# Optimization experiments

Measured on AMD Instinct MI355X. Metric: run time of the kernel, lower is better.

Reference implementation:

```python
import jax, jax.numpy as jnp
import numpy as np

# ---- model constants (match init_kwargs) ----
B, N = 128, 4096                 # N_BATCH, N_NEURON
N_STEPS, N_STEADY, N_WINDOW = 200, 100, 20
V_THRESH, V_REST = 1.0, 0.0
DT, TAU, TAU_SYN = 0.01, 0.02, 0.02
EXP_DT_TAU = float(np.exp(-DT / TAU))
DT_TAU = DT / TAU
EXP_DT_TAU_SYN = float(np.exp(-DT / TAU_SYN))
DT_TAU_SYN = DT / TAU_SYN

# recording schedule: steps >= N_STEADY with step % N_WINDOW == 0
REC_IDX = np.arange(N_STEADY, N_STEPS, N_WINDOW)                     # [100,120,140,160,180]
PREV_IDX = np.concatenate([[N_STEADY - N_WINDOW - 1], REC_IDX[:-1]])  # window starts (exclusive)


def setup_inputs() -> dict:
    key = jax.random.key(0)
    k1, k2, k3 = jax.random.split(key, 3)
    # feedforward drive with a positive baseline so the net actually spikes
    ff_input = 0.5 + 0.3 * jax.random.normal(k1, (B, N_STEPS, N), jnp.float32)
    # recurrent weights (transposed, as in torch: spikes @ Wab_T)
    Wab_T = jax.random.normal(k2, (N, N), jnp.float32) / np.sqrt(N)
    # initial synaptic recurrent input (torch initVolt uses randn)
    rec0 = jax.random.normal(k3, (B, N), jnp.float32)
    return {"ff_input": ff_input, "Wab_T": Wab_T, "rec0": rec0}


def reference(ff_input, Wab_T, rec0):
    dtype = ff_input.dtype
    volts0 = jnp.zeros((B, N), dtype)
    spikes0 = jnp.zeros((B, N), dtype)  # volts=0 < V_THRESH -> no initial spikes

    def step(carry, ff_t):
        volts, rec, spikes = carry
        hidden = spikes @ Wab_T                              # [B,N] GEMM
        rec = rec * EXP_DT_TAU_SYN + hidden * DT_TAU_SYN     # synaptic decay (SYN_DYN)
        volts = volts * EXP_DT_TAU + DT_TAU * (ff_t + rec)   # LIF voltage update
        spk = volts >= V_THRESH
        volts = jnp.where(spk, V_REST, volts)                # masked reset
        spikes = spk.astype(dtype)
        return (volts, rec, spikes), (spikes, volts)

    _, (spk_all, v_all) = jax.lax.scan(
        step, (volts0, rec0, spikes0), jnp.swapaxes(ff_input, 0, 1)
    )  # spk_all, v_all: [N_STEPS, B, N]

    # windowed moving averages, matching torch accumulate/reset logic
    cs_s = jnp.cumsum(spk_all, axis=0)
    cs_v = jnp.cumsum(v_all, axis=0)
    rates = (cs_s[REC_IDX] - cs_s[PREV_IDX]) / N_WINDOW      # [5, B, N]
    volts_avg = (cs_v[REC_IDX] - cs_v[PREV_IDX]) / N_WINDOW
    spikes_rec = spk_all[REC_IDX]

    return (
        jnp.swapaxes(rates, 0, 1),       # [B, 5, N]
        jnp.swapaxes(volts_avg, 0, 1),   # [B, 5, N]
        jnp.swapaxes(spikes_rec, 0, 1),  # [B, 5, N]
    )
```

## Files before the change

kernel.cpp:

```cpp
#include <hip/hip_runtime.h>
#include <stdint.h>

#define NBATCH 128
#define NNEUR  4096
#define TLAST  180
#define DECAY  0.6065306597126334f

__global__ __launch_bounds__(256) void lif_step(
    const float* __restrict__ ff, const float* __restrict__ W,
    const float* __restrict__ rec0, float* __restrict__ out,
    float* __restrict__ volts, float* __restrict__ rec,
    float* __restrict__ sum_s, float* __restrict__ sum_v,
    const unsigned long long* __restrict__ bits_old,
    unsigned long long* __restrict__ bits_new, int t)
{
#pragma clang fp contract(off)
    __shared__ __align__(16) unsigned short slist[NNEUR];
    __shared__ int scnt;

    const int tid  = threadIdx.x;
    const int lane = tid & 63;
    const int wid  = tid >> 6;
    const int bid  = blockIdx.x;
    const int b    = bid >> 3;
    const int tile = bid & 7;
    const int c0   = (tile << 9) + (wid << 7);
    const int n0   = c0 + (lane << 1);
    const unsigned laneb = (unsigned)n0 * 4u;

    float accx = 0.f, accy = 0.f;

    if (t > 0) {
        if (wid == 0) {
            unsigned long long m = bits_old[(b << 6) + lane];
            int c = __popcll(m);
            int x = c;
            #pragma unroll
            for (int o = 1; o < 64; o <<= 1) {
                int y = __shfl_up(x, (unsigned)o);
                if (lane >= o) x += y;
            }
            if (lane == 63) scnt = x;
            int widx = x - c;
            const int jb = ((lane >> 1) << 7) + (lane & 1);
            while (m) {
                int u = __builtin_ctzll(m);
                m &= m - 1;
                slist[widx++] = (unsigned short)(jb + (u << 1));
            }
        }
        __syncthreads();

        const int cnt = scnt;
        const char* Wb = (const char*)W;

        auto load8 = [&](float2* R, int ii) {
            const uint4 pk = *(const uint4*)(slist + ii);
            unsigned q[4];
            q[0] = pk.x; q[1] = pk.y; q[2] = pk.z; q[3] = pk.w;
            #pragma unroll
            for (int k = 0; k < 4; ++k) {
                const unsigned qq = __builtin_amdgcn_readfirstlane(q[k]);
                R[2 * k]     = *(const float2*)(Wb + (((qq & 0xffffu) << 14) + laneb));
                R[2 * k + 1] = *(const float2*)(Wb + (((qq >> 16)     << 14) + laneb));
            }
        };
        auto acc8 = [&](const float2* R) {
            #pragma unroll
            for (int k = 0; k < 8; ++k) { accx += R[k].x; accy += R[k].y; }
        };

        int i = 0;
        if (cnt >= 8) {
            float2 A[8], B[8];
            load8(A, 0); i = 8;
            while (i + 16 <= cnt) {
                load8(B, i);     acc8(A);
                load8(A, i + 8); acc8(B);
                i += 16;
            }
            if (i + 8 <= cnt) { load8(B, i); acc8(A); acc8(B); i += 8; }
            else              { acc8(A); }
        }
        for (; i < cnt; ++i) {
            unsigned q = (unsigned)slist[i];
            q = __builtin_amdgcn_readfirstlane(q);
            const float2 w = *(const float2*)(Wb + ((q << 14) + laneb));
            accx += w.x; accy += w.y;
        }
    }

    const size_t idx = ((size_t)b << 12) + (size_t)n0;

    float2 r2 = (t == 0) ? *(const float2*)(rec0 + idx)
                         : *(const float2*)(rec + idx);
    r2.x = r2.x * DECAY + accx * 0.5f;
    r2.y = r2.y * DECAY + accy * 0.5f;

    const float2 f2 = *(const float2*)(ff + (((size_t)b * 200 + (size_t)t) << 12) + n0);

    float2 v2 = make_float2(0.f, 0.f);
    if (t > 0) v2 = *(const float2*)(volts + idx);
    v2.x = v2.x * DECAY + 0.5f * (f2.x + r2.x);
    v2.y = v2.y * DECAY + 0.5f * (f2.y + r2.y);

    const bool s0 = v2.x >= 1.0f, s1 = v2.y >= 1.0f;
    if (s0) v2.x = 0.f;
    if (s1) v2.y = 0.f;

    *(float2*)(volts + idx) = v2;
    *(float2*)(rec + idx)   = r2;

    const unsigned long long m0 = __ballot(s0), m1 = __ballot(s1);
    if (lane == 0) {
        unsigned long long* dst = bits_new + (b << 6) + ((c0 >> 7) << 1);
        dst[0] = m0; dst[1] = m1;
    }

    if (t >= 80) {
        const float2 s2 = make_float2(s0 ? 1.f : 0.f, s1 ? 1.f : 0.f);
        const bool start = (t == 80) || (t == 101) || (t == 121) || (t == 141) || (t == 161);
        float2 ss, sv;
        if (start) {
            ss = s2; sv = v2;
        } else {
            ss = *(const float2*)(sum_s + idx);
            sv = *(const float2*)(sum_v + idx);
            ss.x += s2.x; ss.y += s2.y;
            sv.x += v2.x; sv.y += v2.y;
        }
        *(float2*)(sum_s + idx) = ss;
        *(float2*)(sum_v + idx) = sv;

        if (t >= 100 && ((t - 100) % 20) == 0) {
            const int k = (t - 100) / 20;
            const size_t oidx = (((size_t)b * 5 + (size_t)k) << 12) + n0;
            float* rates = out;
            float* vavg  = out + (size_t)NBATCH * 5 * NNEUR;
            float* srec  = out + (size_t)NBATCH * 5 * NNEUR * 2;
            *(float2*)(rates + oidx) = make_float2(ss.x / 20.f, ss.y / 20.f);
            *(float2*)(vavg  + oidx) = make_float2(sv.x / 20.f, sv.y / 20.f);
            *(float2*)(srec  + oidx) = s2;
        }
    }
}

extern "C" void kernel_launch(void* const* d_in, const int* in_sizes, int n_in,
                              void* d_out, int out_size, void* d_ws, size_t ws_size,
                              hipStream_t stream) {
    const float* ff   = (const float*)d_in[0];
    const float* W    = (const float*)d_in[1];
    const float* rec0 = (const float*)d_in[2];
    float* out = (float*)d_out;

    char* ws = (char*)d_ws;
    const size_t STATE = (size_t)NBATCH * NNEUR * sizeof(float);
    float* volts = (float*)(ws);
    float* rec   = (float*)(ws + STATE);
    float* sum_s = (float*)(ws + 2 * STATE);
    float* sum_v = (float*)(ws + 3 * STATE);
    unsigned long long* bits = (unsigned long long*)(ws + 4 * STATE);
    const int BWORDS = NBATCH * (NNEUR / 64);

    for (int t = 0; t <= TLAST; ++t) {
        lif_step<<<dim3(1024), dim3(256), 0, stream>>>(
            ff, W, rec0, out, volts, rec, sum_s, sum_v,
            bits + (size_t)(t & 1) * BWORDS,
            bits + (size_t)((t + 1) & 1) * BWORDS, t);
    }
}
```

Measured before the change: 3.721 ms.

## Fuse all timesteps into one persistent kernel with pairwise block flag sync

```diff
diff --git a/kernel.cpp b/kernel.cpp
--- a/kernel.cpp
+++ b/kernel.cpp
@@ -5,14 +5,17 @@
 #define NNEUR  4096
 #define TLAST  180
 #define DECAY  0.6065306597126334f
+#define SCOPE  __HIP_MEMORY_SCOPE_AGENT
 
-__global__ __launch_bounds__(256) void lif_step(
+__global__ void lif_init(unsigned* flags) {
+    flags[threadIdx.x * 32] = 0u;
+}
+
+__global__ __launch_bounds__(1024, 1) void lif_pair(
     const float* __restrict__ ff, const float* __restrict__ W,
     const float* __restrict__ rec0, float* __restrict__ out,
-    float* __restrict__ volts, float* __restrict__ rec,
-    float* __restrict__ sum_s, float* __restrict__ sum_v,
-    const unsigned long long* __restrict__ bits_old,
-    unsigned long long* __restrict__ bits_new, int t)
+    unsigned long long* __restrict__ bits,
+    unsigned* __restrict__ flags)
 {
 #pragma clang fp contract(off)
     __shared__ __align__(16) unsigned short slist[NNEUR];
@@ -22,125 +25,140 @@
     const int lane = tid & 63;
     const int wid  = tid >> 6;
     const int bid  = blockIdx.x;
-    const int b    = bid >> 3;
-    const int tile = bid & 7;
-    const int c0   = (tile << 9) + (wid << 7);
-    const int n0   = c0 + (lane << 1);
+    const int b    = bid & 127;
+    const int g    = bid >> 7;
+    const int n0   = (g << 11) + (tid << 1);
     const unsigned laneb = (unsigned)n0 * 4u;
 
-    float accx = 0.f, accy = 0.f;
+    unsigned* myflag   = flags + bid * 32;
+    unsigned* partflag = flags + (bid ^ 128) * 32;
 
-    if (t > 0) {
-        if (wid == 0) {
-            unsigned long long m = bits_old[(b << 6) + lane];
-            int c = __popcll(m);
-            int x = c;
-            #pragma unroll
-            for (int o = 1; o < 64; o <<= 1) {
-                int y = __shfl_up(x, (unsigned)o);
-                if (lane >= o) x += y;
+    const char*  Wb   = (const char*)W;
+    const float* fptr = ff + (((size_t)b * 200) << 12) + n0;
+    const size_t idx  = ((size_t)b << 12) + (size_t)n0;
+
+    float2 v2 = make_float2(0.f, 0.f);
+    float2 r2 = *(const float2*)(rec0 + idx);
+    float2 ss = v2, sv = v2;
+
+    for (int t = 0; t <= TLAST; ++t) {
+        const float2 f2 = *(const float2*)fptr;
+        fptr += NNEUR;
+
+        float accx = 0.f, accy = 0.f;
+        if (t > 0) {
+            if (tid == 0) {
+                while ((int)__hip_atomic_load(partflag, __ATOMIC_ACQUIRE, SCOPE) < t)
+                    __builtin_amdgcn_s_sleep(2);
             }
-            if (lane == 63) scnt = x;
-            int widx = x - c;
-            const int jb = ((lane >> 1) << 7) + (lane & 1);
-            while (m) {
-                int u = __builtin_ctzll(m);
-                m &= m - 1;
-                slist[widx++] = (unsigned short)(jb + (u << 1));
+            __syncthreads();
+
+            const unsigned long long* bsrc =
+                bits + (((size_t)((t - 1) & 1)) << 13) + (b << 6);
+            if (wid == 0) {
+                unsigned long long m =
+                    __hip_atomic_load(&bsrc[lane], __ATOMIC_RELAXED, SCOPE);
+                const int c = __popcll(m);
+                int x = c;
+                #pragma unroll
+                for (int o = 1; o < 64; o <<= 1) {
+                    int y = __shfl_up(x, (unsigned)o);
+                    if (lane >= o) x += y;
+                }
+                if (lane == 63) scnt = x;
+                int widx = x - c;
+                const int jb = ((lane >> 1) << 7) + (lane & 1);
+                while (m) {
+                    const int u = __builtin_ctzll(m);
+                    m &= m - 1;
+                    slist[widx++] = (unsigned short)(jb + (u << 1));
+                }
+            }
+            __syncthreads();
+
+            const int cnt = scnt;
+            auto load8 = [&](float2* R, int ii) {
+                const uint4 pk = *(const uint4*)(slist + ii);
+                unsigned q[4];
+                q[0] = pk.x; q[1] = pk.y; q[2] = pk.z; q[3] = pk.w;
+                #pragma unroll
+                for (int k = 0; k < 4; ++k) {
+                    const unsigned qq = __builtin_amdgcn_readfirstlane(q[k]);
+                    R[2 * k]     = *(const float2*)(Wb + (((qq & 0xffffu) << 14) + laneb));
+                    R[2 * k + 1] = *(const float2*)(Wb + (((qq >> 16)     << 14) + laneb));
+                }
+            };
+            auto acc8 = [&](const float2* R) {
+                #pragma unroll
+                for (int k = 0; k < 8; ++k) { accx += R[k].x; accy += R[k].y; }
+            };
+
+            int i = 0;
+            if (cnt >= 8) {
+                float2 A[8], B[8];
+                load8(A, 0); i = 8;
+                while (i + 16 <= cnt) {
+                    load8(B, i);     acc8(A);
+                    load8(A, i + 8); acc8(B);
+                    i += 16;
+                }
+                if (i + 8 <= cnt) { load8(B, i); acc8(A); acc8(B); i += 8; }
+                else              { acc8(A); }
+            }
+            for (; i < cnt; ++i) {
+                unsigned q = (unsigned)slist[i];
+                q = __builtin_amdgcn_readfirstlane(q);
+                const float2 wv = *(const float2*)(Wb + ((q << 14) + laneb));
+                accx += wv.x; accy += wv.y;
             }
         }
-        __syncthreads();
 
-        const int cnt = scnt;
-        const char* Wb = (const char*)W;
+        r2.x = r2.x * DECAY + accx * 0.5f;
+        r2.y = r2.y * DECAY + accy * 0.5f;
 
-        auto load8 = [&](float2* R, int ii) {
-            const uint4 pk = *(const uint4*)(slist + ii);
-            unsigned q[4];
-            q[0] = pk.x; q[1] = pk.y; q[2] = pk.z; q[3] = pk.w;
-            #pragma unroll
-            for (int k = 0; k < 4; ++k) {
-                const unsigned qq = __builtin_amdgcn_readfirstlane(q[k]);
-                R[2 * k]     = *(const float2*)(Wb + (((qq & 0xffffu) << 14) + laneb));
-                R[2 * k + 1] = *(const float2*)(Wb + (((qq >> 16)     << 14) + laneb));
+        v2.x = v2.x * DECAY + 0.5f * (f2.x + r2.x);
+        v2.y = v2.y * DECAY + 0.5f * (f2.y + r2.y);
+
+        const bool s0 = v2.x >= 1.0f, s1 = v2.y >= 1.0f;
+        if (s0) v2.x = 0.f;
+        if (s1) v2.y = 0.f;
+
+        const unsigned long long m0 = __ballot(s0), m1 = __ballot(s1);
+        if (t < TLAST) {
+            if (lane == 0) {
+                unsigned long long* dst =
+                    bits + (((size_t)(t & 1)) << 13) + (b << 6) + (g << 5) + (wid << 1);
+                __hip_atomic_store(&dst[0], m0, __ATOMIC_RELAXED, SCOPE);
+                __hip_atomic_store(&dst[1], m1, __ATOMIC_RELAXED, SCOPE);
             }
-        };
-        auto acc8 = [&](const float2* R) {
-            #pragma unroll
-            for (int k = 0; k < 8; ++k) { accx += R[k].x; accy += R[k].y; }
-        };
+        }
 
-        int i = 0;
-        if (cnt >= 8) {
-            float2 A[8], B[8];
-            load8(A, 0); i = 8;
-            while (i + 16 <= cnt) {
-                load8(B, i);     acc8(A);
-                load8(A, i + 8); acc8(B);
-                i += 16;
+        if (t >= 80) {
+            const float2 s2 = make_float2(s0 ? 1.f : 0.f, s1 ? 1.f : 0.f);
+            const bool start = (t == 80) || (t == 101) || (t == 121) ||
+                               (t == 141) || (t == 161);
+            if (start) {
+                ss = s2; sv = v2;
+            } else {
+                ss.x += s2.x; ss.y += s2.y;
+                sv.x += v2.x; sv.y += v2.y;
             }
-            if (i + 8 <= cnt) { load8(B, i); acc8(A); acc8(B); i += 8; }
-            else              { acc8(A); }
+            if (t == 100 || t == 120 || t == 140 || t == 160 || t == 180) {
+                const int k = (t - 100) / 20;
+                const size_t oidx = (((size_t)b * 5 + (size_t)k) << 12) + n0;
+                float* rates = out;
+                float* vavg  = out + (size_t)NBATCH * 5 * NNEUR;
+                float* srec  = out + (size_t)NBATCH * 5 * NNEUR * 2;
+                *(float2*)(rates + oidx) = make_float2(ss.x / 20.f, ss.y / 20.f);
+                *(float2*)(vavg  + oidx) = make_float2(sv.x / 20.f, sv.y / 20.f);
+                *(float2*)(srec  + oidx) = s2;
+            }
         }
-        for (; i < cnt; ++i) {
-            unsigned q = (unsigned)slist[i];
-            q = __builtin_amdgcn_readfirstlane(q);
-            const float2 w = *(const float2*)(Wb + ((q << 14) + laneb));
-            accx += w.x; accy += w.y;
-        }
-    }
 
-    const size_t idx = ((size_t)b << 12) + (size_t)n0;
-
-    float2 r2 = (t == 0) ? *(const float2*)(rec0 + idx)
-                         : *(const float2*)(rec + idx);
-    r2.x = r2.x * DECAY + accx * 0.5f;
-    r2.y = r2.y * DECAY + accy * 0.5f;
-
-    const float2 f2 = *(const float2*)(ff + (((size_t)b * 200 + (size_t)t) << 12) + n0);
-
-    float2 v2 = make_float2(0.f, 0.f);
-    if (t > 0) v2 = *(const float2*)(volts + idx);
-    v2.x = v2.x * DECAY + 0.5f * (f2.x + r2.x);
-    v2.y = v2.y * DECAY + 0.5f * (f2.y + r2.y);
-
-    const bool s0 = v2.x >= 1.0f, s1 = v2.y >= 1.0f;
-    if (s0) v2.x = 0.f;
-    if (s1) v2.y = 0.f;
-
-    *(float2*)(volts + idx) = v2;
-    *(float2*)(rec + idx)   = r2;
-
-    const unsigned long long m0 = __ballot(s0), m1 = __ballot(s1);
-    if (lane == 0) {
-        unsigned long long* dst = bits_new + (b << 6) + ((c0 >> 7) << 1);
-        dst[0] = m0; dst[1] = m1;
-    }
-
-    if (t >= 80) {
-        const float2 s2 = make_float2(s0 ? 1.f : 0.f, s1 ? 1.f : 0.f);
-        const bool start = (t == 80) || (t == 101) || (t == 121) || (t == 141) || (t == 161);
-        float2 ss, sv;
-        if (start) {
-            ss = s2; sv = v2;
-        } else {
-            ss = *(const float2*)(sum_s + idx);
-            sv = *(const float2*)(sum_v + idx);
-            ss.x += s2.x; ss.y += s2.y;
-            sv.x += v2.x; sv.y += v2.y;
-        }
-        *(float2*)(sum_s + idx) = ss;
-        *(float2*)(sum_v + idx) = sv;
-
-        if (t >= 100 && ((t - 100) % 20) == 0) {
-            const int k = (t - 100) / 20;
-            const size_t oidx = (((size_t)b * 5 + (size_t)k) << 12) + n0;
-            float* rates = out;
-            float* vavg  = out + (size_t)NBATCH * 5 * NNEUR;
-            float* srec  = out + (size_t)NBATCH * 5 * NNEUR * 2;
-            *(float2*)(rates + oidx) = make_float2(ss.x / 20.f, ss.y / 20.f);
-            *(float2*)(vavg  + oidx) = make_float2(sv.x / 20.f, sv.y / 20.f);
-            *(float2*)(srec  + oidx) = s2;
+        if (t < TLAST) {
+            __syncthreads();
+            if (tid == 0)
+                __hip_atomic_store(myflag, (unsigned)(t + 1), __ATOMIC_RELEASE, SCOPE);
         }
     }
 }
@@ -154,18 +172,9 @@
     float* out = (float*)d_out;
 
     char* ws = (char*)d_ws;
-    const size_t STATE = (size_t)NBATCH * NNEUR * sizeof(float);
-    float* volts = (float*)(ws);
-    float* rec   = (float*)(ws + STATE);
-    float* sum_s = (float*)(ws + 2 * STATE);
-    float* sum_v = (float*)(ws + 3 * STATE);
-    unsigned long long* bits = (unsigned long long*)(ws + 4 * STATE);
-    const int BWORDS = NBATCH * (NNEUR / 64);
+    unsigned long long* bits = (unsigned long long*)ws;
+    unsigned* flags = (unsigned*)(ws + 2 * 8192 * sizeof(unsigned long long));
 
-    for (int t = 0; t <= TLAST; ++t) {
-        lif_step<<<dim3(1024), dim3(256), 0, stream>>>(
-            ff, W, rec0, out, volts, rec, sum_s, sum_v,
-            bits + (size_t)(t & 1) * BWORDS,
-            bits + (size_t)((t + 1) & 1) * BWORDS, t);
-    }
+    lif_init<<<dim3(1), dim3(256), 0, stream>>>(flags);
+    lif_pair<<<dim3(256), dim3(1024), 0, stream>>>(ff, W, rec0, out, bits, flags);
 }
```

New measurement: 5.468 ms. +47.0%, slower.
